# Kernel optimization log

Hardware: AMD Instinct MI355X
Metric: run time of the kernel (lower is better)

The kernel has to match this reference:

```python
import jax, jax.numpy as jnp
import numpy as np

B, S = 16, 2048
VOCAB, N_KINGS = 32000, 27
D_EMB, D_MODEL = 256, 512
LN_EPS = 1e-5

def setup_inputs() -> dict:
    key = jax.random.key(0)
    ks = jax.random.split(key, 8)
    sequence = jax.random.randint(ks[0], (B, S), 0, VOCAB)
    king_id = jax.random.randint(ks[1], (B, 1), 0, N_KINGS)
    # stacked per-king token embedding tables (replaces dict-dispatched nn.Embedding modules)
    token_tables = jax.random.normal(ks[2], (N_KINGS, VOCAB, D_EMB), dtype=jnp.float32) * 0.02
    # nn.Bilinear(d_embedding, d_embedding, d_model): weight [M, E1, E2], bias [M]
    Wb = jax.random.normal(ks[3], (D_MODEL, D_EMB, D_EMB), dtype=jnp.float32) * (1.0 / np.sqrt(D_EMB))
    bb = jax.random.normal(ks[4], (D_MODEL,), dtype=jnp.float32) * 0.01
    king_table = jax.random.normal(ks[5], (N_KINGS, D_EMB), dtype=jnp.float32) * 0.02
    gamma = jnp.ones((D_MODEL,), dtype=jnp.float32)
    beta = jnp.zeros((D_MODEL,), dtype=jnp.float32)
    return {"sequence": sequence, "king_id": king_id, "token_tables": token_tables,
            "Wb": Wb, "bb": bb, "king_table": king_table, "gamma": gamma, "beta": beta}

def reference(sequence, king_id, token_tables, Wb, bb, king_table, gamma, beta):
    k = king_id[:, 0]                                  # [B]
    # batched dispatch: per-sample king-specific token embedding -> [B, S, E]
    tok = token_tables[k[:, None], sequence]
    kemb = king_table[k]                               # [B, E]
    # Bilinear(tok, kemb_repeated): kemb is constant over s, so contract it first.
    Wk = jnp.einsum('mij,bj->bmi', Wb, kemb)           # [B, M, E]
    x = jnp.einsum('bsi,bmi->bsm', tok, Wk) + bb       # [B, S, M]
    # LayerNorm over d_model
    mean = jnp.mean(x, axis=-1, keepdims=True)
    var = jnp.mean(jnp.square(x - mean), axis=-1, keepdims=True)
    return (x - mean) * jax.lax.rsqrt(var + LN_EPS) * gamma + beta
```

## Files before the change

kernel.cpp:

```cpp
#include <hip/hip_runtime.h>
#include <hip/hip_bf16.h>

#define B 16
#define S 2048
#define VOCAB 32000
#define D_EMB 256
#define D_MODEL 512
#define LN_EPS 1e-5f

using bf16x8 = __attribute__((ext_vector_type(8))) short;
using f32x4  = __attribute__((ext_vector_type(4))) float;

static __device__ __forceinline__ unsigned short f2bf(float f) {
    __hip_bfloat16 h = __float2bfloat16(f);
    return *reinterpret_cast<unsigned short*>(&h);
}

static __device__ __forceinline__ bf16x8 pack8(f32x4 v0, f32x4 v1) {
    union { unsigned short us[8]; bf16x8 v; } pk;
    pk.us[0] = f2bf(v0.x); pk.us[1] = f2bf(v0.y);
    pk.us[2] = f2bf(v0.z); pk.us[3] = f2bf(v0.w);
    pk.us[4] = f2bf(v1.x); pk.us[5] = f2bf(v1.y);
    pk.us[6] = f2bf(v1.z); pk.us[7] = f2bf(v1.w);
    return pk.v;
}

__global__ __launch_bounds__(256) void wk_mfma(
    const float* __restrict__ Wb,
    const float* __restrict__ king_table,
    const int* __restrict__ king_id,
    unsigned short* __restrict__ Wk)
{
    const int t    = threadIdx.x;
    const int lane = t & 63;
    const int wave = t >> 6;
    const int lr   = lane & 15;
    const int kg   = lane >> 4;

    const int kid = king_id[lr];
    const float* kp = king_table + (size_t)kid * D_EMB + kg * 8;
    bf16x8 bemb[8];
#pragma unroll
    for (int step = 0; step < 8; ++step) {
        f32x4 v0 = *(const f32x4*)(kp + step * 32);
        f32x4 v1 = *(const f32x4*)(kp + step * 32 + 4);
        bemb[step] = pack8(v0, v1);
    }

    const int rbase = (blockIdx.x * 4 + wave) * 64;

#pragma unroll
    for (int mf = 0; mf < 4; ++mf) {
        const float* arow = Wb + (size_t)(rbase + mf * 16 + lr) * D_EMB + kg * 8;
        f32x4 acc = {};
#pragma unroll
        for (int step = 0; step < 8; ++step) {
            f32x4 v0 = *(const f32x4*)(arow + step * 32);
            f32x4 v1 = *(const f32x4*)(arow + step * 32 + 4);
            acc = __builtin_amdgcn_mfma_f32_16x16x32_bf16(
                pack8(v0, v1), bemb[step], acc, 0, 0, 0);
        }
        union { unsigned short us[4]; uint2 q; } st;
        st.us[0] = f2bf(acc[0]); st.us[1] = f2bf(acc[1]);
        st.us[2] = f2bf(acc[2]); st.us[3] = f2bf(acc[3]);
        *(uint2*)(Wk + (size_t)lr * (D_MODEL * D_EMB) + rbase + mf * 16 + kg * 4) = st.q;
    }
}

#define TSB 64

__global__ __launch_bounds__(512) void gemm_ln_mfma(
    const int* __restrict__ seq,
    const int* __restrict__ king_id,
    const float* __restrict__ token_tables,
    const unsigned short* __restrict__ Wk,
    const float* __restrict__ bb,
    const float* __restrict__ gamma,
    const float* __restrict__ beta,
    float* __restrict__ out)
{
    __shared__ unsigned short tokL[TSB][264];
    __shared__ float red_sum[8][TSB];
    __shared__ float red_sq[8][TSB];
    __shared__ float stats[2][TSB];

    const int b    = blockIdx.y;
    const int s0   = blockIdx.x * TSB;
    const int t    = threadIdx.x;
    const int lane = t & 63;
    const int wave = t >> 6;
    const int lr   = lane & 15;
    const int kg   = lane >> 4;

    const int kb = king_id[b];
    const float* ttab = token_tables + (size_t)kb * VOCAB * D_EMB;

    {
        int row = t >> 3;
        int ck  = (t & 7) * 32;
        int tokidx = seq[b * S + s0 + row];
        const float4* src = (const float4*)(ttab + (size_t)tokidx * D_EMB + ck);
#pragma unroll
        for (int u = 0; u < 4; ++u) {
            float4 v0 = src[u * 2 + 0];
            float4 v1 = src[u * 2 + 1];
            union { unsigned short us[8]; uint4 q; } pk;
            pk.us[0] = f2bf(v0.x); pk.us[1] = f2bf(v0.y);
            pk.us[2] = f2bf(v0.z); pk.us[3] = f2bf(v0.w);
            pk.us[4] = f2bf(v1.x); pk.us[5] = f2bf(v1.y);
            pk.us[6] = f2bf(v1.z); pk.us[7] = f2bf(v1.w);
            *(uint4*)&tokL[row][ck + u * 8] = pk.q;
        }
    }
    __syncthreads();

    const int m0 = wave * 64;
    const uint4* aptr[4];
    const uint4* bptr[4];
#pragma unroll
    for (int mf = 0; mf < 4; ++mf)
        aptr[mf] = (const uint4*)&tokL[mf * 16 + lr][kg * 8];
#pragma unroll
    for (int nf = 0; nf < 4; ++nf) {
        int col = m0 + nf * 16 + lr;
        bptr[nf] = (const uint4*)(Wk + ((size_t)(b * D_MODEL + col)) * D_EMB + kg * 8);
    }

    f32x4 acc[4][4] = {};

#pragma unroll
    for (int step = 0; step < 8; ++step) {
        bf16x8 af[4], bfr[4];
#pragma unroll
        for (int mf = 0; mf < 4; ++mf) {
            uint4 q = aptr[mf][step * 4];
            af[mf] = __builtin_bit_cast(bf16x8, q);
        }
#pragma unroll
        for (int nf = 0; nf < 4; ++nf) {
            uint4 q = bptr[nf][step * 4];
            bfr[nf] = __builtin_bit_cast(bf16x8, q);
        }
#pragma unroll
        for (int mf = 0; mf < 4; ++mf)
#pragma unroll
            for (int nf = 0; nf < 4; ++nf)
                acc[mf][nf] = __builtin_amdgcn_mfma_f32_16x16x32_bf16(
                    af[mf], bfr[nf], acc[mf][nf], 0, 0, 0);
    }

    float bbv[4], gv[4], bv[4];
#pragma unroll
    for (int nf = 0; nf < 4; ++nf) {
        int col = m0 + nf * 16 + lr;
        bbv[nf] = bb[col];
        gv[nf]  = gamma[col];
        bv[nf]  = beta[col];
    }

#pragma unroll
    for (int mf = 0; mf < 4; ++mf) {
#pragma unroll
        for (int r = 0; r < 4; ++r) {
            float sum = 0.0f, sq = 0.0f;
#pragma unroll
            for (int nf = 0; nf < 4; ++nf) {
                float v = acc[mf][nf][r] + bbv[nf];
                acc[mf][nf][r] = v;
                sum += v;
                sq  += v * v;
            }
#pragma unroll
            for (int off = 1; off < 16; off <<= 1) {
                sum += __shfl_xor(sum, off);
                sq  += __shfl_xor(sq, off);
            }
            if (lr == 0) {
                int row = mf * 16 + kg * 4 + r;
                red_sum[wave][row] = sum;
                red_sq[wave][row]  = sq;
            }
        }
    }
    __syncthreads();

    if (t < TSB) {
        float s = 0.0f, q = 0.0f;
#pragma unroll
        for (int w = 0; w < 8; ++w) { s += red_sum[w][t]; q += red_sq[w][t]; }
        float mean = s * (1.0f / D_MODEL);
        float var  = q * (1.0f / D_MODEL) - mean * mean;
        stats[0][t] = mean;
        stats[1][t] = rsqrtf(var + LN_EPS);
    }
    __syncthreads();

#pragma unroll
    for (int mf = 0; mf < 4; ++mf) {
#pragma unroll
        for (int r = 0; r < 4; ++r) {
            int row = mf * 16 + kg * 4 + r;
            float mean = stats[0][row];
            float rstd = stats[1][row];
            float* op = out + ((size_t)b * S + s0 + row) * D_MODEL + m0 + lr;
#pragma unroll
            for (int nf = 0; nf < 4; ++nf)
                op[nf * 16] = (acc[mf][nf][r] - mean) * rstd * gv[nf] + bv[nf];
        }
    }
}

extern "C" void kernel_launch(void* const* d_in, const int* in_sizes, int n_in,
                              void* d_out, int out_size, void* d_ws, size_t ws_size,
                              hipStream_t stream)
{
    const int*   seq          = (const int*)d_in[0];
    const int*   king_id      = (const int*)d_in[1];
    const float* token_tables = (const float*)d_in[2];
    const float* Wb           = (const float*)d_in[3];
    const float* bb           = (const float*)d_in[4];
    const float* king_table   = (const float*)d_in[5];
    const float* gamma        = (const float*)d_in[6];
    const float* beta         = (const float*)d_in[7];
    float* out = (float*)d_out;

    unsigned short* Wk = (unsigned short*)d_ws;

    wk_mfma<<<dim3((D_MODEL * D_EMB) / 256), dim3(256), 0, stream>>>(
        Wb, king_table, king_id, Wk);
    gemm_ln_mfma<<<dim3(S / TSB, B), dim3(512), 0, stream>>>(
        seq, king_id, token_tables, Wk, bb, gamma, beta, out);
}
```

Measured before the change: 68.73 us.

## Stage Wk K-slices through shared memory with register prefetch in GEMM-LN kernel

Replaces direct global loads of the Wk operand inside the MFMA loop with a cooperative stage of one 32-wide K slice of Wk (all 512 output columns) into LDS per step. The next slice is prefetched into registers while the current one is consumed. It also adds a min-blocks hint to the launch bounds. This trades per-wave redundant global/L2 reads for coalesced block-wide loads, at the cost of 16 extra barriers per block, 32KB more LDS, and a tighter register budget.

```diff
diff --git a/kernel.cpp b/kernel.cpp
--- a/kernel.cpp
+++ b/kernel.cpp
@@ -69,7 +69,7 @@
 
 #define TSB 64
 
-__global__ __launch_bounds__(512) void gemm_ln_mfma(
+__global__ __launch_bounds__(512, 4) void gemm_ln_mfma(
     const int* __restrict__ seq,
     const int* __restrict__ king_id,
     const float* __restrict__ token_tables,
@@ -80,6 +80,7 @@
     float* __restrict__ out)
 {
     __shared__ unsigned short tokL[TSB][264];
+    __shared__ unsigned short wkq[D_MODEL * 32];
     __shared__ float red_sum[8][TSB];
     __shared__ float red_sq[8][TSB];
     __shared__ float stats[2][TSB];
@@ -94,6 +95,15 @@
 
     const int kb = king_id[b];
     const float* ttab = token_tables + (size_t)kb * VOCAB * D_EMB;
+    const unsigned short* wkb = Wk + (size_t)b * (D_MODEL * D_EMB);
+
+    const int mrow = t >> 2;
+    const int cc   = t & 3;
+
+    uint4 wst[4];
+#pragma unroll
+    for (int c = 0; c < 4; ++c)
+        wst[c] = *(const uint4*)(wkb + (size_t)(c * 128 + mrow) * D_EMB + cc * 8);
 
     {
         int row = t >> 3;
@@ -112,33 +122,33 @@
             *(uint4*)&tokL[row][ck + u * 8] = pk.q;
         }
     }
+#pragma unroll
+    for (int c = 0; c < 4; ++c)
+        *(uint4*)&wkq[(c * 512 + t) * 8] = wst[c];
     __syncthreads();
 
     const int m0 = wave * 64;
-    const uint4* aptr[4];
-    const uint4* bptr[4];
-#pragma unroll
-    for (int mf = 0; mf < 4; ++mf)
-        aptr[mf] = (const uint4*)&tokL[mf * 16 + lr][kg * 8];
-#pragma unroll
-    for (int nf = 0; nf < 4; ++nf) {
-        int col = m0 + nf * 16 + lr;
-        bptr[nf] = (const uint4*)(Wk + ((size_t)(b * D_MODEL + col)) * D_EMB + kg * 8);
-    }
-
     f32x4 acc[4][4] = {};
 
 #pragma unroll
-    for (int step = 0; step < 8; ++step) {
+    for (int e = 0; e < 8; ++e) {
+        uint4 nst[4];
+        if (e < 7) {
+#pragma unroll
+            for (int c = 0; c < 4; ++c)
+                nst[c] = *(const uint4*)(wkb + (size_t)(c * 128 + mrow) * D_EMB
+                                         + (e + 1) * 32 + cc * 8);
+        }
+
         bf16x8 af[4], bfr[4];
 #pragma unroll
         for (int mf = 0; mf < 4; ++mf) {
-            uint4 q = aptr[mf][step * 4];
+            uint4 q = *(const uint4*)&tokL[mf * 16 + lr][e * 32 + kg * 8];
             af[mf] = __builtin_bit_cast(bf16x8, q);
         }
 #pragma unroll
         for (int nf = 0; nf < 4; ++nf) {
-            uint4 q = bptr[nf][step * 4];
+            uint4 q = *(const uint4*)&wkq[(m0 + nf * 16 + lr) * 32 + kg * 8];
             bfr[nf] = __builtin_bit_cast(bf16x8, q);
         }
 #pragma unroll
@@ -147,6 +157,14 @@
             for (int nf = 0; nf < 4; ++nf)
                 acc[mf][nf] = __builtin_amdgcn_mfma_f32_16x16x32_bf16(
                     af[mf], bfr[nf], acc[mf][nf], 0, 0, 0);
+
+        __syncthreads();
+        if (e < 7) {
+#pragma unroll
+            for (int c = 0; c < 4; ++c)
+                *(uint4*)&wkq[(c * 512 + t) * 8] = nst[c];
+        }
+        __syncthreads();
     }
 
     float bbv[4], gv[4], bv[4];
```

New measurement: 82.67 us. 1.2x slower.
